# Kernel tuning notes

Measured on AMD Instinct MI355X. Metric: run time of the kernel, lower is better.

Reference implementation:

```python
import jax, jax.numpy as jnp
import numpy as np
import math

EMB_S = 64
HEADS = 8
EMB = EMB_S * HEADS  # 512
M = int(EMB_S * 0.5)  # 32 random features
B, T = 8, 4096
EPS = 1e-5


def setup_inputs() -> dict:
    key = jax.random.key(0)
    ks = jax.random.split(key, 16)
    s_in = 1.0 / math.sqrt(EMB_S)
    s_emb = 1.0 / math.sqrt(EMB)
    s_hid = 1.0 / math.sqrt(4 * EMB)
    return {
        "x": jax.random.normal(ks[0], (B, T, EMB), jnp.float32),
        "w": jax.random.normal(ks[1], (M, EMB_S), jnp.float32),  # frozen random features
        "kqv_w": jax.random.uniform(ks[2], (3 * EMB_S, EMB_S), jnp.float32, -s_in, s_in),
        "kqv_b": jax.random.uniform(ks[3], (3 * EMB_S,), jnp.float32, -s_in, s_in),
        "proj_w": jax.random.uniform(ks[4], (EMB, EMB), jnp.float32, -s_emb, s_emb),
        "proj_b": jax.random.uniform(ks[5], (EMB,), jnp.float32, -s_emb, s_emb),
        "ln1_g": 1.0 + 0.02 * jax.random.normal(ks[6], (EMB,), jnp.float32),
        "ln1_b": 0.02 * jax.random.normal(ks[7], (EMB,), jnp.float32),
        "ln2_g": 1.0 + 0.02 * jax.random.normal(ks[8], (EMB,), jnp.float32),
        "ln2_b": 0.02 * jax.random.normal(ks[9], (EMB,), jnp.float32),
        "mlp_w1": jax.random.uniform(ks[10], (4 * EMB, EMB), jnp.float32, -s_emb, s_emb),
        "mlp_b1": jax.random.uniform(ks[11], (4 * EMB,), jnp.float32, -s_emb, s_emb),
        "mlp_w2": jax.random.uniform(ks[12], (EMB, 4 * EMB), jnp.float32, -s_hid, s_hid),
        "mlp_b2": jax.random.uniform(ks[13], (EMB,), jnp.float32, -s_hid, s_hid),
    }


def _layer_norm(x, g, b):
    mu = jnp.mean(x, axis=-1, keepdims=True)
    var = jnp.mean(jnp.square(x - mu), axis=-1, keepdims=True)
    return (x - mu) * jax.lax.rsqrt(var + EPS) * g + b


def _prm_exp(z, w):
    # z: [B,T,H,E]; softmax-kernel random features, [B,T,H,M]
    xd = 0.5 * jnp.sum(z * z, axis=-1, keepdims=True)
    wtx = jnp.einsum("bthe,me->bthm", z, w)
    return jnp.exp(wtx - xd) / math.sqrt(M)


def reference(x, w, kqv_w, kqv_b, proj_w, proj_b, ln1_g, ln1_b, ln2_g, ln2_b,
              mlp_w1, mlp_b1, mlp_w2, mlp_b2):
    Bb, Tt, _ = x.shape
    h = _layer_norm(x, ln1_g, ln1_b).reshape(Bb, Tt, HEADS, EMB_S)
    kqv = jnp.einsum("bthe,fe->bthf", h, kqv_w) + kqv_b  # [B,T,H,3E]
    k, q, v = jnp.split(kqv, 3, axis=-1)  # torch.split order: k, q, v
    kp = _prm_exp(k, w)  # [B,T,H,M]
    qp = _prm_exp(q, w)
    D = jnp.einsum("bthm,bhm->bth", qp, kp.sum(axis=1))  # [B,T,H]
    kptv = jnp.einsum("bthe,bthm->bhem", v, kp)  # [B,H,E,M]
    y = jnp.einsum("bthm,bhem->bthe", qp, kptv) / D[..., None]
    y = y.reshape(Bb, Tt, EMB)
    attn = jnp.einsum("btf,ef->bte", y, proj_w) + proj_b  # dropout = identity (eval)
    x = x + attn
    h2 = _layer_norm(x, ln2_g, ln2_b)
    hid = jax.nn.gelu(jnp.einsum("bte,fe->btf", h2, mlp_w1) + mlp_b1, approximate=False)
    mlp_out = jnp.einsum("btf,ef->bte", hid, mlp_w2) + mlp_b2
    return x + mlp_out
```

## Files before the change

kernel.cpp:

```cpp
#include <hip/hip_runtime.h>
#include <hip/hip_bf16.h>

typedef __bf16 bf16x8_t __attribute__((ext_vector_type(8)));
typedef float f32x4_t __attribute__((ext_vector_type(4)));
using bf16 = __hip_bfloat16;

#define EMB 512
#define NTOK 32768
#define NROW 262144
#define SQRT_M_INV 0.17677669529663687f
#define KNC 16

__device__ __forceinline__ void gload16(const void* g, void* l) {
  __builtin_amdgcn_global_load_lds((const __attribute__((address_space(1))) void*)g,
                                   (__attribute__((address_space(3))) void*)l, 16, 0, 0);
}

template <int N> __device__ __forceinline__ void wait_vm_lgkm0() {
  asm volatile("s_waitcnt vmcnt(%0) lgkmcnt(0)" :: "n"(N) : "memory");
  __builtin_amdgcn_sched_barrier(0);
}

__device__ __forceinline__ float fast_gelu(float v) {
  float u = v * 0.70710678118654752f;
  float a = fabsf(u);
  float tt = __builtin_amdgcn_rcpf(fmaf(0.3275911f, a, 1.0f));
  float p = fmaf(tt, 1.061405429f, -1.453152027f);
  p = fmaf(tt, p, 1.421413741f);
  p = fmaf(tt, p, -0.284496736f);
  p = fmaf(tt, p, 0.254829592f);
  p = p * tt;
  float e = __expf(-a * a);
  float er = fmaf(-p, e, 1.0f);
  er = copysignf(er, u);
  return 0.5f * v * (1.0f + er);
}

__device__ __forceinline__ void cvt4(const float* __restrict__ in,
                                     bf16* __restrict__ out, int i4, int n4) {
  if (i4 < n4) {
    float4 v = ((const float4*)in)[i4];
    alignas(8) bf16 o[4];
    o[0] = __float2bfloat16(v.x); o[1] = __float2bfloat16(v.y);
    o[2] = __float2bfloat16(v.z); o[3] = __float2bfloat16(v.w);
    *(uint2*)(out + i4 * 4) = *(const uint2*)o;
  }
}
__global__ __launch_bounds__(256) void f2b4_kernel(
    const float* __restrict__ a, bf16* __restrict__ oa, int na4,
    const float* __restrict__ b, bf16* __restrict__ ob, int nb4,
    const float* __restrict__ c, bf16* __restrict__ oc, int nc4,
    const float* __restrict__ d, bf16* __restrict__ od, int nd4) {
  int i4 = blockIdx.x * 256 + threadIdx.x;
  cvt4(a, oa, i4, na4);
  cvt4(b, ob, i4, nb4);
  cvt4(c, oc, i4, nc4);
  cvt4(d, od, i4, nd4);
}

__global__ __launch_bounds__(256) void ln_kernel(const float* __restrict__ x,
                                                 const float* __restrict__ g,
                                                 const float* __restrict__ bt,
                                                 bf16* __restrict__ out) {
  int lane = threadIdx.x & 63;
  int row = blockIdx.x * 4 + (threadIdx.x >> 6);
  const float* xr = x + (size_t)row * EMB;
  float4 v0 = ((const float4*)xr)[lane * 2];
  float4 v1 = ((const float4*)xr)[lane * 2 + 1];
  float s = v0.x + v0.y + v0.z + v0.w + v1.x + v1.y + v1.z + v1.w;
#pragma unroll
  for (int o = 32; o; o >>= 1) s += __shfl_xor(s, o);
  float mu = s * (1.0f / 512.0f);
  float vs = 0.f, d;
  d = v0.x - mu; vs += d * d;  d = v0.y - mu; vs += d * d;
  d = v0.z - mu; vs += d * d;  d = v0.w - mu; vs += d * d;
  d = v1.x - mu; vs += d * d;  d = v1.y - mu; vs += d * d;
  d = v1.z - mu; vs += d * d;  d = v1.w - mu; vs += d * d;
#pragma unroll
  for (int o = 32; o; o >>= 1) vs += __shfl_xor(vs, o);
  float rstd = rsqrtf(vs * (1.0f / 512.0f) + 1e-5f);
  float4 g0 = ((const float4*)g)[lane * 2], g1 = ((const float4*)g)[lane * 2 + 1];
  float4 b0 = ((const float4*)bt)[lane * 2], b1 = ((const float4*)bt)[lane * 2 + 1];
  alignas(16) bf16 o8[8];
  o8[0] = __float2bfloat16((v0.x - mu) * rstd * g0.x + b0.x);
  o8[1] = __float2bfloat16((v0.y - mu) * rstd * g0.y + b0.y);
  o8[2] = __float2bfloat16((v0.z - mu) * rstd * g0.z + b0.z);
  o8[3] = __float2bfloat16((v0.w - mu) * rstd * g0.w + b0.w);
  o8[4] = __float2bfloat16((v1.x - mu) * rstd * g1.x + b1.x);
  o8[5] = __float2bfloat16((v1.y - mu) * rstd * g1.y + b1.y);
  o8[6] = __float2bfloat16((v1.z - mu) * rstd * g1.z + b1.z);
  o8[7] = __float2bfloat16((v1.w - mu) * rstd * g1.w + b1.w);
  *(uint4*)(out + (size_t)row * EMB + lane * 8) = *(const uint4*)o8;
}

template <int BM, int BN, int WM, int WN, int OP>
__global__ __launch_bounds__(256) void gemm_bt(const bf16* __restrict__ A,
                                               const bf16* __restrict__ W,
                                               const float* __restrict__ bias,
                                               const float* __restrict__ res,
                                               float* __restrict__ outF,
                                               bf16* __restrict__ outB,
                                               int M, int N, int K) {
  constexpr int BK = 32;
  constexpr int TM = BM / WM, TN = BN / WN;
  constexpr int NI = TM / 16, NJ = TN / 16;
  constexpr int AP = BM * BK / 2048;
  constexpr int WP = BN * BK / 2048;
  constexpr int LPT = AP + WP;
  alignas(16) __shared__ bf16 As[3][BM * BK];
  alignas(16) __shared__ bf16 Ws[3][BN * BK];
  int t = threadIdx.x;
  int lane = t & 63, wid = t >> 6;
  int wm = wid % WM, wn = wid / WM;
  int nwg = gridDim.x * gridDim.y;
  int lin = blockIdx.y * gridDim.x + blockIdx.x;
  if ((nwg & 7) == 0) lin = (lin & 7) * (nwg >> 3) + (lin >> 3);
  int bn = (lin % gridDim.x) * BN, bm = (lin / gridDim.x) * BM;
  int lr = lane & 15, lq = lane >> 4;

  const int r0 = t >> 2;
  const int c0lin = (t & 3) * 8;
  const int sc = (r0 >> 1) & 3;
  const int c0g = ((t & 3) ^ sc) * 8;
  const int rsw = (lq ^ ((lr >> 1) & 3)) * 8;

  const bf16* ap = A + (size_t)(bm + r0) * K + c0g;
  const bf16* wp = W + (size_t)(bn + r0) * K + c0g;
  const size_t strA = (size_t)64 * K;

  f32x4_t acc[NI][NJ];
#pragma unroll
  for (int i = 0; i < NI; ++i)
#pragma unroll
    for (int j = 0; j < NJ; ++j)
#pragma unroll
      for (int r = 0; r < 4; ++r) acc[i][j][r] = 0.f;

  auto stage = [&](int buf) {
#pragma unroll
    for (int p = 0; p < AP; ++p)
      gload16(ap + (size_t)p * strA, &As[buf][(r0 + p * 64) * BK + c0lin]);
#pragma unroll
    for (int p = 0; p < WP; ++p)
      gload16(wp + (size_t)p * strA, &Ws[buf][(r0 + p * 64) * BK + c0lin]);
    ap += BK;
    wp += BK;
  };
  auto compute = [&](int buf) {
    bf16x8_t afr[NI], bfr[NJ];
#pragma unroll
    for (int i = 0; i < NI; ++i)
      afr[i] = *(const bf16x8_t*)&As[buf][(wm * TM + i * 16 + lr) * BK + rsw];
#pragma unroll
    for (int j = 0; j < NJ; ++j)
      bfr[j] = *(const bf16x8_t*)&Ws[buf][(wn * TN + j * 16 + lr) * BK + rsw];
#pragma unroll
    for (int i = 0; i < NI; ++i)
#pragma unroll
      for (int j = 0; j < NJ; ++j)
        acc[i][j] = __builtin_amdgcn_mfma_f32_16x16x32_bf16(afr[i], bfr[j], acc[i][j], 0, 0, 0);
  };

  const int nt = K / BK;
  stage(0);
  stage(1);
  int bc = 0, bs = 2;
  for (int kt = 0; kt < nt - 2; ++kt) {
    wait_vm_lgkm0<LPT>();
    __builtin_amdgcn_s_barrier();
    __builtin_amdgcn_sched_barrier(0);
    stage(bs);
    compute(bc);
    bc = (bc == 2) ? 0 : bc + 1;
    bs = (bs == 2) ? 0 : bs + 1;
  }
  wait_vm_lgkm0<LPT>();
  __builtin_amdgcn_s_barrier();
  __builtin_amdgcn_sched_barrier(0);
  compute(bc);
  bc = (bc == 2) ? 0 : bc + 1;
  wait_vm_lgkm0<0>();
  __builtin_amdgcn_s_barrier();
  __builtin_amdgcn_sched_barrier(0);
  compute(bc);

#pragma unroll
  for (int i = 0; i < NI; ++i)
#pragma unroll
    for (int j = 0; j < NJ; ++j) {
      int gn = bn + wn * TN + j * 16 + lr;
      float bv = bias[gn];
#pragma unroll
      for (int r = 0; r < 4; ++r) {
        int gm = bm + wm * TM + i * 16 + lq * 4 + r;
        float v = acc[i][j][r] + bv;
        size_t off = (size_t)gm * N + gn;
        if (OP == 0) {
          outF[off] = v;
        } else if (OP == 1) {
          outF[off] = v + res[off];
        } else {
          outB[off] = __float2bfloat16(fast_gelu(v));
        }
      }
    }
}

__device__ __forceinline__ size_t bh_row(size_t grow) {
  size_t h = grow & 7, bt = grow >> 3;
  size_t b = bt >> 12, tt = bt & 4095;
  return ((b * 8 + h) << 12) + tt;
}

__global__ __launch_bounds__(256) void kqv_prm_kernel(
    const bf16* __restrict__ A,
    const bf16* __restrict__ Wk,
    const float* __restrict__ bias,
    const float* __restrict__ wrf,
    float* __restrict__ kp, float* __restrict__ qp,
    bf16* __restrict__ vout) {
  constexpr int LDZ = 136;
  constexpr int LDV = 72;
  alignas(16) __shared__ char u_raw[27648];
  bf16* As  = (bf16*)u_raw;
  bf16* Ws  = (bf16*)(u_raw + 4096);
  bf16* zkq = (bf16*)u_raw;
  bf16* vs  = (bf16*)(u_raw + 17408);
  float* xd_s = (float*)(u_raw + 26624);

  int t = threadIdx.x;
  int lane = t & 63, wid = t >> 6;
  int wm = wid & 1, wn = wid >> 1;
  int lr = lane & 15, lq = lane >> 4;
  size_t row0 = (size_t)blockIdx.x * 64;

  bf16x8_t wfrag[2][2];
#pragma unroll
  for (int mt = 0; mt < 2; ++mt)
#pragma unroll
    for (int ks = 0; ks < 2; ++ks) {
      const float* src = wrf + (mt * 16 + lr) * 64 + ks * 32 + lq * 8;
#pragma unroll
      for (int jj = 0; jj < 8; ++jj) wfrag[mt][ks][jj] = (__bf16)src[jj];
    }

  f32x4_t acc[2][6];
#pragma unroll
  for (int i = 0; i < 2; ++i)
#pragma unroll
    for (int j = 0; j < 6; ++j)
#pragma unroll
      for (int r = 0; r < 4; ++r) acc[i][j][r] = 0.f;

  const int r0 = t >> 2, c0 = (t * 8) & 31;
  for (int k0 = 0; k0 < 64; k0 += 32) {
    gload16(&A[(row0 + r0) * 64 + k0 + c0], &As[r0 * 32 + c0]);
#pragma unroll
    for (int p = 0; p < 3; ++p) {
      int r = r0 + p * 64;
      gload16(&Wk[(size_t)r * 64 + k0 + c0], &Ws[r * 32 + c0]);
    }
    __syncthreads();
    bf16x8_t af[2], bfr[6];
#pragma unroll
    for (int i = 0; i < 2; ++i)
      af[i] = *(const bf16x8_t*)&As[(wm * 32 + i * 16 + lr) * 32 + lq * 8];
#pragma unroll
    for (int j = 0; j < 6; ++j)
      bfr[j] = *(const bf16x8_t*)&Ws[(wn * 96 + j * 16 + lr) * 32 + lq * 8];
#pragma unroll
    for (int i = 0; i < 2; ++i)
#pragma unroll
      for (int j = 0; j < 6; ++j)
        acc[i][j] = __builtin_amdgcn_mfma_f32_16x16x32_bf16(af[i], bfr[j], acc[i][j], 0, 0, 0);
    __syncthreads();
  }

#pragma unroll
  for (int i = 0; i < 2; ++i)
#pragma unroll
    for (int j = 0; j < 6; ++j) {
      int col = wn * 96 + j * 16 + lr;
      float bv = bias[col];
      int rowb = wm * 32 + i * 16 + lq * 4;
#pragma unroll
      for (int r = 0; r < 4; ++r) {
        float v = acc[i][j][r] + bv;
        if (col < 128) zkq[(rowb + r) * LDZ + col] = __float2bfloat16(v);
        else           vs[(rowb + r) * LDV + (col - 128)] = __float2bfloat16(v);
      }
    }
  __syncthreads();

  if (t < 128) {
    int r = t & 63, sel = t >> 6;
    const bf16* zr = &zkq[r * LDZ + sel * 64];
    float xd = 0.f;
#pragma unroll
    for (int c = 0; c < 64; c += 8) {
      bf16x8_t z8 = *(const bf16x8_t*)&zr[c];
#pragma unroll
      for (int jj = 0; jj < 8; ++jj) { float f = (float)z8[jj]; xd += f * f; }
    }
    xd_s[r * 2 + sel] = 0.5f * xd;
  }
  __syncthreads();

#pragma unroll
  for (int p = 0; p < 2; ++p) {
    int idx = t + p * 256;
    int r = idx >> 3, c8 = idx & 7;
    size_t nr = bh_row(row0 + r);
    *(uint4*)&vout[nr * 64 + c8 * 8] = *(const uint4*)&vs[r * LDV + c8 * 8];
  }

  int sel = wn;
  f32x4_t aw[2][2];
#pragma unroll
  for (int i = 0; i < 2; ++i)
#pragma unroll
    for (int mt = 0; mt < 2; ++mt)
#pragma unroll
      for (int r = 0; r < 4; ++r) aw[i][mt][r] = 0.f;
#pragma unroll
  for (int ks = 0; ks < 2; ++ks) {
    bf16x8_t af2[2];
#pragma unroll
    for (int i = 0; i < 2; ++i)
      af2[i] = *(const bf16x8_t*)&zkq[(wm * 32 + i * 16 + lr) * LDZ + sel * 64 + ks * 32 + lq * 8];
#pragma unroll
    for (int i = 0; i < 2; ++i)
#pragma unroll
      for (int mt = 0; mt < 2; ++mt)
        aw[i][mt] = __builtin_amdgcn_mfma_f32_16x16x32_bf16(af2[i], wfrag[mt][ks], aw[i][mt], 0, 0, 0);
  }
  float* outp = sel ? qp : kp;
#pragma unroll
  for (int i = 0; i < 2; ++i)
#pragma unroll
    for (int r = 0; r < 4; ++r) {
      int row = wm * 32 + i * 16 + lq * 4 + r;
      size_t nr = bh_row(row0 + row);
#pragma unroll
      for (int mt = 0; mt < 2; ++mt) {
        int m = mt * 16 + lr;
        outp[nr * 32 + m] =
            __expf(aw[i][mt][r] - xd_s[row * 2 + sel]) * SQRT_M_INV;
      }
    }
}

__global__ __launch_bounds__(256) void kptv_kernel(const bf16* __restrict__ v2,
                                                   const float* __restrict__ kp2,
                                                   float* __restrict__ part) {
  int bh = blockIdx.x, chunk = blockIdx.y;
  int t = threadIdx.x;
  int ts = t >> 6;
  int eg = (t >> 2) & 15;
  int g  = t & 3;
  const int T0 = chunk * 256;
  const bf16* vp = v2 + ((size_t)bh * 4096 + T0) * 64 + eg * 4;
  const float* kpp = kp2 + ((size_t)bh * 4096 + T0) * 32 + g * 8;

  float acc[4][8];
  float accs[8];
#pragma unroll
  for (int e = 0; e < 4; ++e)
#pragma unroll
    for (int m = 0; m < 8; ++m) acc[e][m] = 0.f;
#pragma unroll
  for (int m = 0; m < 8; ++m) accs[m] = 0.f;

#pragma unroll 2
  for (int tok = ts; tok < 256; tok += 4) {
    union { uint2 u; ushort s[4]; } vr;
    vr.u = *(const uint2*)(vp + (size_t)tok * 64);
    float ve[4];
#pragma unroll
    for (int e = 0; e < 4; ++e)
      ve[e] = __uint_as_float((uint32_t)vr.s[e] << 16);
    float4 k0 = *(const float4*)(kpp + (size_t)tok * 32);
    float4 k1 = *(const float4*)(kpp + (size_t)tok * 32 + 4);
    float km[8] = {k0.x, k0.y, k0.z, k0.w, k1.x, k1.y, k1.z, k1.w};
#pragma unroll
    for (int e = 0; e < 4; ++e)
#pragma unroll
      for (int m = 0; m < 8; ++m) acc[e][m] = fmaf(ve[e], km[m], acc[e][m]);
#pragma unroll
    for (int m = 0; m < 8; ++m) accs[m] += km[m];
  }

  __shared__ float red[256][33];
  __shared__ float reds[4][4][8];
#pragma unroll
  for (int e = 0; e < 4; ++e)
#pragma unroll
    for (int m = 0; m < 8; ++m) red[t][e * 8 + m] = acc[e][m];
  if (eg == 0) {
#pragma unroll
    for (int m = 0; m < 8; ++m) reds[ts][g][m] = accs[m];
  }
  __syncthreads();

  int l = t >> 2, q = t & 3;
  int leg = l >> 2, lg = l & 3;
  float o[8];
#pragma unroll
  for (int m = 0; m < 8; ++m)
    o[m] = red[l][q * 8 + m] + red[l + 64][q * 8 + m] +
           red[l + 128][q * 8 + m] + red[l + 192][q * 8 + m];
  float* pp = part + (size_t)(bh * KNC + chunk) * 2080 + (leg * 4 + q) * 32 + lg * 8;
  *(float4*)pp = make_float4(o[0], o[1], o[2], o[3]);
  *(float4*)(pp + 4) = make_float4(o[4], o[5], o[6], o[7]);
  if (t < 32) {
    int g2 = t >> 3, j = t & 7;
    float s = reds[0][g2][j] + reds[1][g2][j] + reds[2][g2][j] + reds[3][g2][j];
    part[(size_t)(bh * KNC + chunk) * 2080 + 2048 + g2 * 8 + j] = s;
  }
}

__global__ __launch_bounds__(256) void y_kernel(const float* __restrict__ qp2,
                                                const float* __restrict__ part,
                                                bf16* __restrict__ y) {
  int bh = blockIdx.x, chunk = blockIdx.y;
  int b = bh >> 3, h = bh & 7;
  __shared__ float kv_s[64][36];
  __shared__ float ks_s[32];
  __shared__ float inv_dd[512];
  alignas(16) __shared__ float qp_s[2][16][32];
  int t = threadIdx.x;
  int e = t & 63, iq = t >> 6;
  const int T0 = chunk * 512;
  const size_t qbase = (size_t)bh * 4096 + T0;

  {
    int er = t >> 2, m0 = (t & 3) * 8;
    float4 a0 = make_float4(0.f, 0.f, 0.f, 0.f);
    float4 a1 = make_float4(0.f, 0.f, 0.f, 0.f);
#pragma unroll 4
    for (int c = 0; c < KNC; ++c) {
      const float* pp = part + (size_t)(bh * KNC + c) * 2080 + er * 32 + m0;
      float4 u = *(const float4*)pp;
      float4 v = *(const float4*)(pp + 4);
      a0.x += u.x; a0.y += u.y; a0.z += u.z; a0.w += u.w;
      a1.x += v.x; a1.y += v.y; a1.z += v.z; a1.w += v.w;
    }
    *(float4*)&kv_s[er][m0] = a0;
    *(float4*)&kv_s[er][m0 + 4] = a1;
    if (t < 32) {
      float s = 0.f;
#pragma unroll 4
      for (int c = 0; c < KNC; ++c)
        s += part[(size_t)(bh * KNC + c) * 2080 + 2048 + t];
      ks_s[t] = s;
    }
  }
  __syncthreads();

  float kv[32];
#pragma unroll
  for (int m = 0; m < 32; m += 4) *(float4*)&kv[m] = *(const float4*)&kv_s[e][m];

  if (t < 128)
    gload16(qp2 + (qbase + (t >> 3)) * 32 + (t & 7) * 4,
            &qp_s[0][t >> 3][(t & 7) * 4]);

  {
    float ks[32];
#pragma unroll
    for (int m = 0; m < 32; m += 4) *(float4*)&ks[m] = *(const float4*)&ks_s[m];
#pragma unroll
    for (int p = 0; p < 2; ++p) {
      int tok = t + p * 256;
      const float* qrow = qp2 + (qbase + tok) * 32;
      float dd = 0.f;
#pragma unroll
      for (int m = 0; m < 32; m += 4) {
        float4 qq = *(const float4*)&qrow[m];
        dd += qq.x * ks[m] + qq.y * ks[m + 1] + qq.z * ks[m + 2] + qq.w * ks[m + 3];
      }
      inv_dd[tok] = 1.0f / dd;
    }
  }

  float dreg[4];
  int cur = 0;
  for (int grp = 0; grp < 32; ++grp) {
    __syncthreads();
    if (grp > 0) {
      int tokp = (grp - 1) * 16 + iq * 4;
#pragma unroll
      for (int i0 = 0; i0 < 4; ++i0)
        y[(size_t)(b * 4096 + T0 + tokp + i0) * EMB + h * 64 + e] =
            __float2bfloat16(dreg[i0]);
    }
    if (grp < 31 && t < 128) {
      int nr = (grp + 1) * 16;
      gload16(qp2 + (qbase + nr + (t >> 3)) * 32 + (t & 7) * 4,
              &qp_s[cur ^ 1][t >> 3][(t & 7) * 4]);
    }
#pragma unroll
    for (int i0 = 0; i0 < 4; ++i0) {
      int i = iq * 4 + i0;
      float dot = 0.f;
#pragma unroll
      for (int m = 0; m < 32; m += 4) {
        float4 qq = *(const float4*)&qp_s[cur][i][m];
        dot += qq.x * kv[m] + qq.y * kv[m + 1] + qq.z * kv[m + 2] + qq.w * kv[m + 3];
      }
      dreg[i0] = dot * inv_dd[grp * 16 + i];
    }
    cur ^= 1;
  }
#pragma unroll
  for (int i0 = 0; i0 < 4; ++i0) {
    int tokp = 31 * 16 + iq * 4 + i0;
    y[(size_t)(b * 4096 + T0 + tokp) * EMB + h * 64 + e] =
        __float2bfloat16(dreg[i0]);
  }
}

extern "C" void kernel_launch(void* const* d_in, const int* in_sizes, int n_in,
                              void* d_out, int out_size, void* d_ws, size_t ws_size,
                              hipStream_t stream) {
  const float* x      = (const float*)d_in[0];
  const float* w      = (const float*)d_in[1];
  const float* kqv_w  = (const float*)d_in[2];
  const float* kqv_b  = (const float*)d_in[3];
  const float* proj_w = (const float*)d_in[4];
  const float* proj_b = (const float*)d_in[5];
  const float* ln1_g  = (const float*)d_in[6];
  const float* ln1_b  = (const float*)d_in[7];
  const float* ln2_g  = (const float*)d_in[8];
  const float* ln2_b  = (const float*)d_in[9];
  const float* mlp_w1 = (const float*)d_in[10];
  const float* mlp_b1 = (const float*)d_in[11];
  const float* mlp_w2 = (const float*)d_in[12];
  const float* mlp_b2 = (const float*)d_in[13];
  float* out = (float*)d_out;

  char* ws = (char*)d_ws;
  size_t off = 0;
  auto alloc = [&](size_t bytes) -> void* {
    void* p = ws + off;
    off = (off + bytes + 255) & ~(size_t)255;
    return p;
  };

  bf16* kqv_wb  = (bf16*)alloc(12288 * 2);
  bf16* proj_wb = (bf16*)alloc(262144 * 2);
  bf16* w1b     = (bf16*)alloc(1048576 * 2);
  bf16* w2b     = (bf16*)alloc(1048576 * 2);
  bf16* hb      = (bf16*)alloc((size_t)NTOK * EMB * 2);
  bf16* yb      = hb;
  float* qpb    = (float*)alloc((size_t)NROW * 32 * 4);
  bf16* h2b     = (bf16*)qpb;
  float* kpb    = (float*)alloc((size_t)NROW * 32 * 4);
  bf16* hidb    = (bf16*)kpb;
  bf16* vb      = (bf16*)alloc((size_t)NROW * 64 * 2);
  float* partb  = (float*)alloc((size_t)64 * KNC * 2080 * 4);

  f2b4_kernel<<<1024, 256, 0, stream>>>(kqv_w, kqv_wb, 12288 / 4,
                                        proj_w, proj_wb, 262144 / 4,
                                        mlp_w1, w1b, 1048576 / 4,
                                        mlp_w2, w2b, 1048576 / 4);

  ln_kernel<<<NTOK / 4, 256, 0, stream>>>(x, ln1_g, ln1_b, hb);

  kqv_prm_kernel<<<NROW / 64, 256, 0, stream>>>(hb, kqv_wb, kqv_b, w, kpb, qpb, vb);

  kptv_kernel<<<dim3(64, KNC), 256, 0, stream>>>(vb, kpb, partb);

  y_kernel<<<dim3(64, 8), 256, 0, stream>>>(qpb, partb, yb);

  gemm_bt<128, 128, 2, 2, 1><<<dim3(4, NTOK / 128), 256, 0, stream>>>(
      yb, proj_wb, proj_b, x, out, nullptr, NTOK, 512, 512);

  ln_kernel<<<NTOK / 4, 256, 0, stream>>>(out, ln2_g, ln2_b, h2b);

  for (int c = 0; c < 2; ++c) {
    const bf16* h2c = h2b + (size_t)c * 16384 * 512;
    float* outc = out + (size_t)c * 16384 * 512;
    gemm_bt<128, 128, 2, 2, 2><<<dim3(16, 128), 256, 0, stream>>>(
        h2c, w1b, mlp_b1, nullptr, nullptr, hidb, 16384, 2048, 512);
    gemm_bt<64, 128, 1, 4, 1><<<dim3(4, 256), 256, 0, stream>>>(
        hidb, w2b, mlp_b2, outc, outc, nullptr, 16384, 512, 2048);
  }
}
```

Baseline: 550.6 us.

## Fuse MLP up-projection, GELU and down-projection into one kernel

Replaces the two MLP GEMM launches per half-batch with a single fused kernel. Each 512-thread block keeps a 64-row h2 tile in LDS, computes 128-wide hidden chunks with GELU into LDS, and accumulates the down-projection in registers, so the hidden activation never goes to global memory. It also adds s_setprio around the MFMA loops in the existing GEMM. In exchange, only 512 blocks run with heavy LDS and register use, W2 fragments are read directly from global memory without LDS staging, and W1 is re-streamed by every block.

After: 696.0 us. 26.4% more time.

```diff
diff --git a/kernel.cpp b/kernel.cpp
--- a/kernel.cpp
+++ b/kernel.cpp
@@ -154,11 +154,13 @@
 #pragma unroll
     for (int j = 0; j < NJ; ++j)
       bfr[j] = *(const bf16x8_t*)&Ws[buf][(wn * TN + j * 16 + lr) * BK + rsw];
+    __builtin_amdgcn_s_setprio(1);
 #pragma unroll
     for (int i = 0; i < NI; ++i)
 #pragma unroll
       for (int j = 0; j < NJ; ++j)
         acc[i][j] = __builtin_amdgcn_mfma_f32_16x16x32_bf16(afr[i], bfr[j], acc[i][j], 0, 0, 0);
+    __builtin_amdgcn_s_setprio(0);
   };
 
   const int nt = K / BK;
@@ -202,6 +204,157 @@
         } else {
           outB[off] = __float2bfloat16(fast_gelu(v));
         }
+      }
+    }
+}
+
+__global__ __launch_bounds__(512, 2) void fused_mlp_kernel(
+    const bf16* __restrict__ h2,
+    const bf16* __restrict__ W1,
+    const float* __restrict__ b1,
+    const bf16* __restrict__ W2,
+    const float* __restrict__ b2,
+    float* __restrict__ out) {
+  constexpr int LDH2 = 520;
+  constexpr int LDHC = 136;
+  alignas(16) __shared__ bf16 h2s[64 * LDH2];
+  alignas(16) __shared__ bf16 w1s[3][128 * 64];
+  alignas(16) __shared__ bf16 hidc[64 * LDHC];
+
+  int t = threadIdx.x;
+  int lane = t & 63, w = t >> 6;
+  int lr = lane & 15, lq = lane >> 4;
+  int nwg = gridDim.x;
+  int lin = blockIdx.x;
+  lin = (lin & 7) * (nwg >> 3) + (lin >> 3);
+  const int bm = lin * 64;
+  const int row_b = w * 16 + lr;
+
+#pragma unroll
+  for (int p = 0; p < 8; ++p) {
+    int row = w * 8 + p;
+    gload16(&h2[(size_t)(bm + row) * 512 + lane * 8], &h2s[row * LDH2]);
+  }
+
+  auto stage_w1 = [&](int buf, int kc, int k0) {
+#pragma unroll
+    for (int p = 0; p < 2; ++p) {
+      int idx = p * 512 + t;
+      int r = idx >> 3, slot = idx & 7;
+      gload16(&W1[(size_t)(kc * 128 + r) * 512 + k0 + ((slot ^ (r & 7)) * 8)],
+              &w1s[buf][idx * 8]);
+    }
+  };
+
+  f32x4_t acc[4][4];
+#pragma unroll
+  for (int i = 0; i < 4; ++i)
+#pragma unroll
+    for (int j = 0; j < 4; ++j)
+#pragma unroll
+      for (int r = 0; r < 4; ++r) acc[i][j][r] = 0.f;
+  float b2v[4];
+#pragma unroll
+  for (int j = 0; j < 4; ++j) b2v[j] = b2[w * 64 + j * 16 + lr];
+
+#pragma unroll 1
+  for (int kc = 0; kc < 16; ++kc) {
+    f32x4_t acc1[4];
+#pragma unroll
+    for (int i = 0; i < 4; ++i)
+#pragma unroll
+      for (int r = 0; r < 4; ++r) acc1[i][r] = 0.f;
+
+    stage_w1(0, kc, 0);
+    stage_w1(1, kc, 64);
+    int bc = 0, bs = 2;
+    auto compute_w1 = [&](int buf, int ks) {
+      bf16x8_t bf[2];
+#pragma unroll
+      for (int s2 = 0; s2 < 2; ++s2)
+        bf[s2] = *(const bf16x8_t*)&w1s[buf][row_b * 64 +
+                      (((s2 * 4 + lq) ^ (row_b & 7)) * 8)];
+      __builtin_amdgcn_s_setprio(1);
+#pragma unroll
+      for (int s2 = 0; s2 < 2; ++s2)
+#pragma unroll
+        for (int i = 0; i < 4; ++i) {
+          bf16x8_t af = *(const bf16x8_t*)&h2s[(i * 16 + lr) * LDH2 +
+                                               ks * 64 + s2 * 32 + lq * 8];
+          acc1[i] = __builtin_amdgcn_mfma_f32_16x16x32_bf16(af, bf[s2], acc1[i], 0, 0, 0);
+        }
+      __builtin_amdgcn_s_setprio(0);
+    };
+#pragma unroll 1
+    for (int ks = 0; ks < 7; ++ks) {
+      wait_vm_lgkm0<2>();
+      __builtin_amdgcn_s_barrier();
+      __builtin_amdgcn_sched_barrier(0);
+      if (ks < 6) {
+        stage_w1(bs, kc, (ks + 2) * 64);
+        bs = (bs == 2) ? 0 : bs + 1;
+      }
+      compute_w1(bc, ks);
+      bc = (bc == 2) ? 0 : bc + 1;
+    }
+    wait_vm_lgkm0<0>();
+    __builtin_amdgcn_s_barrier();
+    __builtin_amdgcn_sched_barrier(0);
+    compute_w1(bc, 7);
+
+    {
+      float b1v = b1[kc * 128 + row_b];
+#pragma unroll
+      for (int i = 0; i < 4; ++i)
+#pragma unroll
+        for (int r = 0; r < 4; ++r) {
+          float v = acc1[i][r] + b1v;
+          hidc[(i * 16 + lq * 4 + r) * LDHC + row_b] = __float2bfloat16(fast_gelu(v));
+        }
+    }
+    __syncthreads();
+
+    {
+      const bf16* w2p = W2 + (size_t)(w * 64) * 2048 + kc * 128 + lq * 8;
+      bf16x8_t b2f[4], b2n[4];
+#pragma unroll
+      for (int j = 0; j < 4; ++j)
+        b2f[j] = *(const bf16x8_t*)(w2p + (size_t)(j * 16 + lr) * 2048);
+#pragma unroll
+      for (int ks = 0; ks < 4; ++ks) {
+        if (ks < 3) {
+#pragma unroll
+          for (int j = 0; j < 4; ++j)
+            b2n[j] = *(const bf16x8_t*)(w2p + (size_t)(j * 16 + lr) * 2048 +
+                                        (ks + 1) * 32);
+        }
+        bf16x8_t af2[4];
+#pragma unroll
+        for (int i = 0; i < 4; ++i)
+          af2[i] = *(const bf16x8_t*)&hidc[(i * 16 + lr) * LDHC + ks * 32 + lq * 8];
+        __builtin_amdgcn_s_setprio(1);
+#pragma unroll
+        for (int i = 0; i < 4; ++i)
+#pragma unroll
+          for (int j = 0; j < 4; ++j)
+            acc[i][j] = __builtin_amdgcn_mfma_f32_16x16x32_bf16(af2[i], b2f[j], acc[i][j], 0, 0, 0);
+        __builtin_amdgcn_s_setprio(0);
+#pragma unroll
+        for (int j = 0; j < 4; ++j) b2f[j] = b2n[j];
+      }
+    }
+  }
+
+#pragma unroll
+  for (int i = 0; i < 4; ++i)
+#pragma unroll
+    for (int j = 0; j < 4; ++j) {
+      int gn = w * 64 + j * 16 + lr;
+#pragma unroll
+      for (int r = 0; r < 4; ++r) {
+        int gm = bm + i * 16 + lq * 4 + r;
+        size_t off = (size_t)gm * 512 + gn;
+        out[off] = acc[i][j][r] + b2v[j] + out[off];
       }
     }
 }
@@ -556,7 +709,6 @@
   float* qpb    = (float*)alloc((size_t)NROW * 32 * 4);
   bf16* h2b     = (bf16*)qpb;
   float* kpb    = (float*)alloc((size_t)NROW * 32 * 4);
-  bf16* hidb    = (bf16*)kpb;
   bf16* vb      = (bf16*)alloc((size_t)NROW * 64 * 2);
   float* partb  = (float*)alloc((size_t)64 * KNC * 2080 * 4);
 
@@ -578,12 +730,5 @@
 
   ln_kernel<<<NTOK / 4, 256, 0, stream>>>(out, ln2_g, ln2_b, h2b);
 
-  for (int c = 0; c < 2; ++c) {
-    const bf16* h2c = h2b + (size_t)c * 16384 * 512;
-    float* outc = out + (size_t)c * 16384 * 512;
-    gemm_bt<128, 128, 2, 2, 2><<<dim3(16, 128), 256, 0, stream>>>(
-        h2c, w1b, mlp_b1, nullptr, nullptr, hidb, 16384, 2048, 512);
-    gemm_bt<64, 128, 1, 4, 1><<<dim3(4, 256), 256, 0, stream>>>(
-        hidb, w2b, mlp_b2, outc, outc, nullptr, 16384, 512, 2048);
-  }
-}
+  fused_mlp_kernel<<<512, 512, 0, stream>>>(h2b, w1b, mlp_b1, w2b, mlp_b2, out);
+}
```
